# Performance work log

Hardware: AMD Instinct MI355X
Metric: run time of the kernel (lower is better)

The kernel has to match this reference:

```python
import jax, jax.numpy as jnp
import numpy as np

B, T, D, SLB = 65536, 50, 17, 30
DROPOUT_RATE = 0.9  # type-3 Gaussian dropout: mask ~ N(1, sqrt((1-p)/p))


def setup_inputs() -> dict:
    key = jax.random.key(0)
    ks = jax.random.split(key, 9)
    p = float(np.sqrt((1.0 - DROPOUT_RATE) / DROPOUT_RATE))
    return {
        "x": jax.random.normal(ks[0], (B, T, D), jnp.float32),
        "W_ih": jax.random.normal(ks[1], (4 * D, D), jnp.float32) * 0.2,
        "W_hh": jax.random.normal(ks[2], (4 * D, D), jnp.float32) * 0.2,
        "b_ih": jax.random.normal(ks[3], (4 * D,), jnp.float32) * 0.1,
        "b_hh": jax.random.normal(ks[4], (4 * D,), jnp.float32) * 0.1,
        "W_lin": jax.random.normal(ks[5], (D, D), jnp.float32) * 0.2,
        "b_lin": jax.random.normal(ks[6], (D,), jnp.float32) * 0.1,
        "mask_ih": 1.0 + p * jax.random.normal(ks[7], (4 * D, D), jnp.float32),
        "mask_hh": 1.0 + p * jax.random.normal(ks[8], (4 * D, D), jnp.float32),
        "step_look_back": SLB,
    }


def reference(x, W_ih, W_hh, b_ih, b_hh, W_lin, b_lin, mask_ih, mask_hh, step_look_back):
    # Masked weights are constant across timesteps (original recomputes the same
    # product each step); transpose once for right-multiplication.
    Wih_t = (W_ih * mask_ih).T   # [D, 4D]
    Whh_t = (W_hh * mask_hh).T   # [H, 4D]
    Wlin_t = W_lin.T             # [H, C]

    x_tbd = jnp.swapaxes(x, 0, 1)          # [T, B, D]
    Bsz = x.shape[0]
    H = W_hh.shape[1]
    h0 = jnp.zeros((Bsz, H), x.dtype)

    def step(carry, inp):
        h, c, prev_out = carry
        x_t, t = inp
        # Teacher-forced input for t < step_look_back, else feed back prediction.
        xi = jnp.where(t < step_look_back, x_t, prev_out)
        gates = xi @ Wih_t + b_ih + h @ Whh_t + b_hh   # [B, 4H]
        i_g, f_g, g_g, o_g = jnp.split(gates, 4, axis=-1)
        c_new = jax.nn.sigmoid(f_g) * c + jax.nn.sigmoid(i_g) * jnp.tanh(g_g)
        h_new = jax.nn.sigmoid(o_g) * jnp.tanh(c_new)
        out = h_new @ Wlin_t + b_lin                    # [B, C]
        return (h_new, c_new, out), out

    Tlen = x.shape[1]
    _, outs = jax.lax.scan(step, (h0, h0, h0), (x_tbd, jnp.arange(Tlen)))
    # Keep only predicted steps: [T - SLB, B, C] -> [B, T - SLB, C]
    return jnp.swapaxes(outs[step_look_back:], 0, 1)
```

## Files before the change

kernel.cpp:

```cpp
#include <hip/hip_runtime.h>


#define Dn 17
#define Gn 68
#define Tn 50
#define WS 68
#define ZS 51
#define HOFF 34

__device__ __forceinline__ float sigm_(float v) {
    float e = __expf(-v);
    return __builtin_amdgcn_rcpf(1.0f + e);
}
__device__ __forceinline__ float tanh_(float v) {
    float e = __expf(2.0f * v);
    return 1.0f - 2.0f * __builtin_amdgcn_rcpf(e + 1.0f);
}
__device__ __forceinline__ float getc(const float4 v, int c) {
    return c == 0 ? v.x : c == 1 ? v.y : c == 2 ? v.z : v.w;
}
__device__ __forceinline__ void fma4(float4& a, float b, const float4 w) {
    a.x = __builtin_fmaf(b, w.x, a.x);
    a.y = __builtin_fmaf(b, w.y, a.y);
    a.z = __builtin_fmaf(b, w.z, a.z);
    a.w = __builtin_fmaf(b, w.w, a.w);
}

__global__ __launch_bounds__(256, 1)
void lstm_fused(const float* __restrict__ x,
                const float* __restrict__ W_ih, const float* __restrict__ W_hh,
                const float* __restrict__ b_ih, const float* __restrict__ b_hh,
                const float* __restrict__ W_lin, const float* __restrict__ b_lin,
                const float* __restrict__ m_ih, const float* __restrict__ m_hh,
                const int* __restrict__ slb_p, float* __restrict__ out)
{
    __shared__ __align__(16) float sWzT[2 * Dn * WS];
    __shared__ __align__(16) float sCzT[Dn * WS];
    __shared__ __align__(16) float sWlT[Dn * 20];
    __shared__ __align__(16) float sBs[WS];
    __shared__ __align__(16) float sBc[WS];
    __shared__ __align__(16) float sBl[20];
    __shared__ float tmpA[Gn * Dn];
    __shared__ float tmpB[Gn * Dn];
    __shared__ float zbuf[256 * ZS];
    __shared__ float obuf[256 * Dn];

    const int tid = threadIdx.x;
    const int b0  = blockIdx.x * 256;

    for (int i = tid; i < Gn * Dn; i += 256) {
        tmpA[i] = W_ih[i] * m_ih[i];
        tmpB[i] = W_hh[i] * m_hh[i];
    }
    for (int i = tid; i < Dn * 20; i += 256) {
        int k = i / 20, m = i - 20 * k;
        sWlT[i] = (m < Dn) ? W_lin[m * Dn + k] : 0.0f;
    }
    if (tid < WS) sBs[tid] = b_ih[tid] + b_hh[tid];
    if (tid < 20) sBl[tid] = (tid < Dn) ? b_lin[tid] : 0.0f;
    __syncthreads();
    for (int i = tid; i < 2 * Dn * WS; i += 256) {
        int k = i / WS, j = i - WS * k;
        sWzT[i] = (k < Dn) ? tmpA[j * Dn + k] : tmpB[j * Dn + (k - Dn)];
    }
    for (int i = tid; i < Dn * WS; i += 256) {
        int k = i / WS, j = i - WS * k;
        float v = tmpB[j * Dn + k];
        #pragma unroll
        for (int m = 0; m < Dn; ++m) v = __builtin_fmaf(tmpA[j * Dn + m], sWlT[k * 20 + m], v);
        sCzT[i] = v;
    }
    if (tid < Gn) {
        float v = sBs[tid];
        #pragma unroll
        for (int m = 0; m < Dn; ++m) v = __builtin_fmaf(tmpA[tid * Dn + m], sBl[m], v);
        sBc[tid] = v;
    }

    #pragma unroll
    for (int e = 0; e < Dn; ++e) zbuf[tid * ZS + HOFF + e] = 0.0f;
    int offx[17], brow_[17], dcol_[17];
    #pragma unroll
    for (int i = 0; i < 17; ++i) {
        int f = tid + 256 * i;
        int br = f / 17, d = f - 17 * br;
        brow_[i] = br; dcol_[i] = d;
        offx[i] = ((b0 + br) * Tn) * Dn + d;
        zbuf[br * ZS + d] = x[offx[i]];
    }
    __syncthreads();

    const int slb = slb_p[0];
    float c[Dn];
    #pragma unroll
    for (int e = 0; e < Dn; ++e) c[e] = 0.0f;
    const float* zr = &zbuf[tid * ZS];
    const float4* bs4 = (const float4*)sBs;

    for (int t = 0; t < slb; ++t) {
        float gx[17];
        const bool pre = (t + 1 < Tn);
        if (pre) {
            #pragma unroll
            for (int i = 0; i < 17; ++i) gx[i] = x[offx[i] + (t + 1) * Dn];
        }
        float4 acc[17];
        #pragma unroll
        for (int j = 0; j < 17; ++j) acc[j] = bs4[j];
        const int xo = (t & 1) * Dn;
        #pragma unroll 2
        for (int k = 0; k < Dn; ++k) {
            float zk = zr[xo + k];
            const float4* w4 = (const float4*)&sWzT[k * WS];
            #pragma unroll
            for (int j = 0; j < 17; ++j) fma4(acc[j], zk, w4[j]);
        }
        #pragma unroll 2
        for (int k = 0; k < Dn; ++k) {
            float zk = zr[HOFF + k];
            const float4* w4 = (const float4*)&sWzT[(Dn + k) * WS];
            #pragma unroll
            for (int j = 0; j < 17; ++j) fma4(acc[j], zk, w4[j]);
        }
        #pragma unroll
        for (int e = 0; e < Dn; ++e) {
            float gi = getc(acc[e >> 2], e & 3);
            float gf = getc(acc[(Dn + e) >> 2], (Dn + e) & 3);
            float gg = getc(acc[(2 * Dn + e) >> 2], (2 * Dn + e) & 3);
            float go = getc(acc[(3 * Dn + e) >> 2], (3 * Dn + e) & 3);
            float cv = __builtin_fmaf(sigm_(gf), c[e], sigm_(gi) * tanh_(gg));
            c[e] = cv;
            zbuf[tid * ZS + HOFF + e] = sigm_(go) * tanh_(cv);
        }
        if (pre) {
            const int xo2 = ((t + 1) & 1) * Dn;
            #pragma unroll
            for (int i = 0; i < 17; ++i) zbuf[brow_[i] * ZS + xo2 + dcol_[i]] = gx[i];
        }
        __syncthreads();
    }

    const int nout = Tn - slb;
    int offo[17];
    #pragma unroll
    for (int i = 0; i < 17; ++i) offo[i] = ((b0 + brow_[i]) * nout) * Dn + dcol_[i];
    const float4* bc4 = (const float4*)sBc;
    const float4* bl4 = (const float4*)sBl;

    for (int tp = 0; tp < nout; ++tp) {
        float4 acc[17];
        #pragma unroll
        for (int j = 0; j < 17; ++j) acc[j] = bc4[j];
        #pragma unroll 2
        for (int k = 0; k < Dn; ++k) {
            float zk = zr[HOFF + k];
            const float4* w4 = (const float4*)&sCzT[k * WS];
            #pragma unroll
            for (int j = 0; j < 17; ++j) fma4(acc[j], zk, w4[j]);
        }
        float hn[Dn];
        #pragma unroll
        for (int e = 0; e < Dn; ++e) {
            float gi = getc(acc[e >> 2], e & 3);
            float gf = getc(acc[(Dn + e) >> 2], (Dn + e) & 3);
            float gg = getc(acc[(2 * Dn + e) >> 2], (2 * Dn + e) & 3);
            float go = getc(acc[(3 * Dn + e) >> 2], (3 * Dn + e) & 3);
            float cv = __builtin_fmaf(sigm_(gf), c[e], sigm_(gi) * tanh_(gg));
            c[e] = cv;
            hn[e] = sigm_(go) * tanh_(cv);
            zbuf[tid * ZS + HOFF + e] = hn[e];
        }
        float4 o4[5];
        #pragma unroll
        for (int j = 0; j < 5; ++j) o4[j] = bl4[j];
        #pragma unroll
        for (int k = 0; k < Dn; ++k) {
            const float4* w4 = (const float4*)&sWlT[k * 20];
            #pragma unroll
            for (int j = 0; j < 5; ++j) fma4(o4[j], hn[k], w4[j]);
        }
        #pragma unroll
        for (int m = 0; m < Dn; ++m) obuf[tid * Dn + m] = getc(o4[m >> 2], m & 3);
        __syncthreads();
        #pragma unroll
        for (int i = 0; i < 17; ++i) out[offo[i] + tp * Dn] = obuf[tid + 256 * i];
        __syncthreads();
    }
}

extern "C" void kernel_launch(void* const* d_in, const int* in_sizes, int n_in,
                              void* d_out, int out_size, void* d_ws, size_t ws_size,
                              hipStream_t stream) {
    (void)in_sizes; (void)n_in; (void)d_ws; (void)ws_size; (void)out_size;
    const float* x     = (const float*)d_in[0];
    const float* W_ih  = (const float*)d_in[1];
    const float* W_hh  = (const float*)d_in[2];
    const float* b_ih  = (const float*)d_in[3];
    const float* b_hh  = (const float*)d_in[4];
    const float* W_lin = (const float*)d_in[5];
    const float* b_lin = (const float*)d_in[6];
    const float* m_ih  = (const float*)d_in[7];
    const float* m_hh  = (const float*)d_in[8];
    const int*   slb   = (const int*)d_in[9];
    float* out = (float*)d_out;

    lstm_fused<<<dim3(256), dim3(256), 0, stream>>>(
        x, W_ih, W_hh, b_ih, b_hh, W_lin, b_lin, m_ih, m_hh, slb, out);
}
```

Baseline: 766.0 us.

## Split weight prep into setup kernel, read weights from global, keep h in registers

```diff
diff --git a/kernel.cpp b/kernel.cpp
--- a/kernel.cpp
+++ b/kernel.cpp
@@ -4,9 +4,16 @@
 #define Dn 17
 #define Gn 68
 #define Tn 50
-#define WS 68
-#define ZS 51
-#define HOFF 34
+
+#define WZ_OFF 0
+#define CZ_OFF 2312
+#define WL_OFF 3468
+#define BS_OFF 3808
+#define BC_OFF 3876
+#define BL_OFF 3944
+#define WS_FLOATS 3964
+
+__device__ __align__(16) float g_ws[WS_FLOATS];
 
 __device__ __forceinline__ float sigm_(float v) {
     float e = __expf(-v);
@@ -26,101 +33,99 @@
     a.w = __builtin_fmaf(b, w.w, a.w);
 }
 
+__global__ void lstm_setup(const float* __restrict__ W_ih, const float* __restrict__ W_hh,
+                           const float* __restrict__ b_ih, const float* __restrict__ b_hh,
+                           const float* __restrict__ W_lin, const float* __restrict__ b_lin,
+                           const float* __restrict__ m_ih, const float* __restrict__ m_hh)
+{
+    __shared__ float A[Gn * Dn];
+    __shared__ float Bm[Gn * Dn];
+    const int tid = threadIdx.x;
+    for (int i = tid; i < Gn * Dn; i += 256) {
+        A[i]  = W_ih[i] * m_ih[i];
+        Bm[i] = W_hh[i] * m_hh[i];
+    }
+    __syncthreads();
+    for (int i = tid; i < 2 * Dn * Gn; i += 256) {
+        int k = i / Gn, j = i - Gn * k;
+        g_ws[WZ_OFF + i] = (k < Dn) ? A[j * Dn + k] : Bm[j * Dn + (k - Dn)];
+    }
+    for (int i = tid; i < Dn * Gn; i += 256) {
+        int k = i / Gn, j = i - Gn * k;
+        float v = Bm[j * Dn + k];
+        for (int m = 0; m < Dn; ++m) v = __builtin_fmaf(A[j * Dn + m], W_lin[m * Dn + k], v);
+        g_ws[CZ_OFF + i] = v;
+    }
+    for (int i = tid; i < Dn * 20; i += 256) {
+        int k = i / 20, m = i - 20 * k;
+        g_ws[WL_OFF + i] = (m < Dn) ? W_lin[m * Dn + k] : 0.0f;
+    }
+    if (tid < Gn) {
+        float bsv = b_ih[tid] + b_hh[tid];
+        g_ws[BS_OFF + tid] = bsv;
+        float v = bsv;
+        for (int m = 0; m < Dn; ++m) v = __builtin_fmaf(A[tid * Dn + m], b_lin[m], v);
+        g_ws[BC_OFF + tid] = v;
+    }
+    if (tid < 20) g_ws[BL_OFF + tid] = (tid < Dn) ? b_lin[tid] : 0.0f;
+}
+
 __global__ __launch_bounds__(256, 1)
-void lstm_fused(const float* __restrict__ x,
-                const float* __restrict__ W_ih, const float* __restrict__ W_hh,
-                const float* __restrict__ b_ih, const float* __restrict__ b_hh,
-                const float* __restrict__ W_lin, const float* __restrict__ b_lin,
-                const float* __restrict__ m_ih, const float* __restrict__ m_hh,
-                const int* __restrict__ slb_p, float* __restrict__ out)
+void lstm_main(const float* __restrict__ x,
+               const int* __restrict__ slb_p, float* __restrict__ out)
 {
-    __shared__ __align__(16) float sWzT[2 * Dn * WS];
-    __shared__ __align__(16) float sCzT[Dn * WS];
-    __shared__ __align__(16) float sWlT[Dn * 20];
-    __shared__ __align__(16) float sBs[WS];
-    __shared__ __align__(16) float sBc[WS];
-    __shared__ __align__(16) float sBl[20];
-    __shared__ float tmpA[Gn * Dn];
-    __shared__ float tmpB[Gn * Dn];
-    __shared__ float zbuf[256 * ZS];
-    __shared__ float obuf[256 * Dn];
+    __shared__ float xbuf[2][256 * Dn];
 
     const int tid = threadIdx.x;
     const int b0  = blockIdx.x * 256;
 
-    for (int i = tid; i < Gn * Dn; i += 256) {
-        tmpA[i] = W_ih[i] * m_ih[i];
-        tmpB[i] = W_hh[i] * m_hh[i];
-    }
-    for (int i = tid; i < Dn * 20; i += 256) {
-        int k = i / 20, m = i - 20 * k;
-        sWlT[i] = (m < Dn) ? W_lin[m * Dn + k] : 0.0f;
-    }
-    if (tid < WS) sBs[tid] = b_ih[tid] + b_hh[tid];
-    if (tid < 20) sBl[tid] = (tid < Dn) ? b_lin[tid] : 0.0f;
+    const float* __restrict__ wz = g_ws + WZ_OFF;
+    const float* __restrict__ cz = g_ws + CZ_OFF;
+    const float* __restrict__ wl = g_ws + WL_OFF;
+    const float4* bs4 = (const float4*)(g_ws + BS_OFF);
+    const float4* bc4 = (const float4*)(g_ws + BC_OFF);
+    const float4* bl4 = (const float4*)(g_ws + BL_OFF);
+
+    int offx[Dn];
+    #pragma unroll
+    for (int i = 0; i < Dn; ++i) {
+        int f  = tid + 256 * i;
+        int br = f / Dn, d = f - Dn * br;
+        offx[i] = ((b0 + br) * Tn) * Dn + d;
+        xbuf[0][f] = x[offx[i]];
+    }
     __syncthreads();
-    for (int i = tid; i < 2 * Dn * WS; i += 256) {
-        int k = i / WS, j = i - WS * k;
-        sWzT[i] = (k < Dn) ? tmpA[j * Dn + k] : tmpB[j * Dn + (k - Dn)];
-    }
-    for (int i = tid; i < Dn * WS; i += 256) {
-        int k = i / WS, j = i - WS * k;
-        float v = tmpB[j * Dn + k];
-        #pragma unroll
-        for (int m = 0; m < Dn; ++m) v = __builtin_fmaf(tmpA[j * Dn + m], sWlT[k * 20 + m], v);
-        sCzT[i] = v;
-    }
-    if (tid < Gn) {
-        float v = sBs[tid];
-        #pragma unroll
-        for (int m = 0; m < Dn; ++m) v = __builtin_fmaf(tmpA[tid * Dn + m], sBl[m], v);
-        sBc[tid] = v;
-    }
-
+
+    const int slb = slb_p[0];
+    float c[Dn], h[Dn];
     #pragma unroll
-    for (int e = 0; e < Dn; ++e) zbuf[tid * ZS + HOFF + e] = 0.0f;
-    int offx[17], brow_[17], dcol_[17];
-    #pragma unroll
-    for (int i = 0; i < 17; ++i) {
-        int f = tid + 256 * i;
-        int br = f / 17, d = f - 17 * br;
-        brow_[i] = br; dcol_[i] = d;
-        offx[i] = ((b0 + br) * Tn) * Dn + d;
-        zbuf[br * ZS + d] = x[offx[i]];
-    }
-    __syncthreads();
-
-    const int slb = slb_p[0];
-    float c[Dn];
-    #pragma unroll
-    for (int e = 0; e < Dn; ++e) c[e] = 0.0f;
-    const float* zr = &zbuf[tid * ZS];
-    const float4* bs4 = (const float4*)sBs;
+    for (int e = 0; e < Dn; ++e) { c[e] = 0.0f; h[e] = 0.0f; }
 
     for (int t = 0; t < slb; ++t) {
-        float gx[17];
-        const bool pre = (t + 1 < Tn);
+        const bool pre = (t + 1 < slb);
+        float gx[Dn];
         if (pre) {
             #pragma unroll
-            for (int i = 0; i < 17; ++i) gx[i] = x[offx[i] + (t + 1) * Dn];
-        }
-        float4 acc[17];
-        #pragma unroll
-        for (int j = 0; j < 17; ++j) acc[j] = bs4[j];
-        const int xo = (t & 1) * Dn;
-        #pragma unroll 2
-        for (int k = 0; k < Dn; ++k) {
-            float zk = zr[xo + k];
-            const float4* w4 = (const float4*)&sWzT[k * WS];
-            #pragma unroll
-            for (int j = 0; j < 17; ++j) fma4(acc[j], zk, w4[j]);
-        }
-        #pragma unroll 2
-        for (int k = 0; k < Dn; ++k) {
-            float zk = zr[HOFF + k];
-            const float4* w4 = (const float4*)&sWzT[(Dn + k) * WS];
-            #pragma unroll
-            for (int j = 0; j < 17; ++j) fma4(acc[j], zk, w4[j]);
+            for (int i = 0; i < Dn; ++i) gx[i] = x[offx[i] + (t + 1) * Dn];
+        }
+        float4 acc[Dn];
+        #pragma unroll
+        for (int j = 0; j < Dn; ++j) acc[j] = bs4[j];
+
+        const float* xr = &xbuf[t & 1][tid * Dn];
+        #pragma unroll
+        for (int k = 0; k < Dn; ++k) {
+            float zk = xr[k];
+            const float4* w4 = (const float4*)(wz + k * Gn);
+            #pragma unroll
+            for (int j = 0; j < Dn; ++j) fma4(acc[j], zk, w4[j]);
+        }
+        #pragma unroll
+        for (int k = 0; k < Dn; ++k) {
+            float zk = h[k];
+            const float4* w4 = (const float4*)(wz + (Dn + k) * Gn);
+            #pragma unroll
+            for (int j = 0; j < Dn; ++j) fma4(acc[j], zk, w4[j]);
         }
         #pragma unroll
         for (int e = 0; e < Dn; ++e) {
@@ -130,35 +135,29 @@
             float go = getc(acc[(3 * Dn + e) >> 2], (3 * Dn + e) & 3);
             float cv = __builtin_fmaf(sigm_(gf), c[e], sigm_(gi) * tanh_(gg));
             c[e] = cv;
-            zbuf[tid * ZS + HOFF + e] = sigm_(go) * tanh_(cv);
+            h[e] = sigm_(go) * tanh_(cv);
         }
         if (pre) {
-            const int xo2 = ((t + 1) & 1) * Dn;
-            #pragma unroll
-            for (int i = 0; i < 17; ++i) zbuf[brow_[i] * ZS + xo2 + dcol_[i]] = gx[i];
+            const int p = (t + 1) & 1;
+            #pragma unroll
+            for (int i = 0; i < Dn; ++i) xbuf[p][tid + 256 * i] = gx[i];
         }
         __syncthreads();
     }
 
-    const int nout = Tn - slb;
-    int offo[17];
-    #pragma unroll
-    for (int i = 0; i < 17; ++i) offo[i] = ((b0 + brow_[i]) * nout) * Dn + dcol_[i];
-    const float4* bc4 = (const float4*)sBc;
-    const float4* bl4 = (const float4*)sBl;
-
+    const int nout  = Tn - slb;
+    const int obase = (b0 + tid) * nout * Dn;
     for (int tp = 0; tp < nout; ++tp) {
-        float4 acc[17];
-        #pragma unroll
-        for (int j = 0; j < 17; ++j) acc[j] = bc4[j];
-        #pragma unroll 2
-        for (int k = 0; k < Dn; ++k) {
-            float zk = zr[HOFF + k];
-            const float4* w4 = (const float4*)&sCzT[k * WS];
-            #pragma unroll
-            for (int j = 0; j < 17; ++j) fma4(acc[j], zk, w4[j]);
-        }
-        float hn[Dn];
+        float4 acc[Dn];
+        #pragma unroll
+        for (int j = 0; j < Dn; ++j) acc[j] = bc4[j];
+        #pragma unroll
+        for (int k = 0; k < Dn; ++k) {
+            float zk = h[k];
+            const float4* w4 = (const float4*)(cz + k * Gn);
+            #pragma unroll
+            for (int j = 0; j < Dn; ++j) fma4(acc[j], zk, w4[j]);
+        }
         #pragma unroll
         for (int e = 0; e < Dn; ++e) {
             float gi = getc(acc[e >> 2], e & 3);
@@ -167,31 +166,27 @@
             float go = getc(acc[(3 * Dn + e) >> 2], (3 * Dn + e) & 3);
             float cv = __builtin_fmaf(sigm_(gf), c[e], sigm_(gi) * tanh_(gg));
             c[e] = cv;
-            hn[e] = sigm_(go) * tanh_(cv);
-            zbuf[tid * ZS + HOFF + e] = hn[e];
+            h[e] = sigm_(go) * tanh_(cv);
         }
         float4 o4[5];
         #pragma unroll
         for (int j = 0; j < 5; ++j) o4[j] = bl4[j];
         #pragma unroll
         for (int k = 0; k < Dn; ++k) {
-            const float4* w4 = (const float4*)&sWlT[k * 20];
-            #pragma unroll
-            for (int j = 0; j < 5; ++j) fma4(o4[j], hn[k], w4[j]);
-        }
-        #pragma unroll
-        for (int m = 0; m < Dn; ++m) obuf[tid * Dn + m] = getc(o4[m >> 2], m & 3);
-        __syncthreads();
-        #pragma unroll
-        for (int i = 0; i < 17; ++i) out[offo[i] + tp * Dn] = obuf[tid + 256 * i];
-        __syncthreads();
+            const float4* w4 = (const float4*)(wl + k * 20);
+            #pragma unroll
+            for (int j = 0; j < 5; ++j) fma4(o4[j], h[k], w4[j]);
+        }
+        float* op = out + obase + tp * Dn;
+        #pragma unroll
+        for (int m = 0; m < Dn; ++m) op[m] = getc(o4[m >> 2], m & 3);
     }
 }
 
 extern "C" void kernel_launch(void* const* d_in, const int* in_sizes, int n_in,
                               void* d_out, int out_size, void* d_ws, size_t ws_size,
                               hipStream_t stream) {
-    (void)in_sizes; (void)n_in; (void)d_ws; (void)ws_size; (void)out_size;
+    (void)in_sizes; (void)n_in; (void)ws_size; (void)out_size; (void)d_ws;
     const float* x     = (const float*)d_in[0];
     const float* W_ih  = (const float*)d_in[1];
     const float* W_hh  = (const float*)d_in[2];
@@ -204,6 +199,7 @@
     const int*   slb   = (const int*)d_in[9];
     float* out = (float*)d_out;
 
-    lstm_fused<<<dim3(256), dim3(256), 0, stream>>>(
-        x, W_ih, W_hh, b_ih, b_hh, W_lin, b_lin, m_ih, m_hh, slb, out);
-}
+    lstm_setup<<<dim3(1), dim3(256), 0, stream>>>(
+        W_ih, W_hh, b_ih, b_hh, W_lin, b_lin, m_ih, m_hh);
+    lstm_main<<<dim3(256), dim3(256), 0, stream>>>(x, slb, out);
+}
```

After: 1.105 ms. 1.44x slower.

## Process two batch rows per thread and keep hidden state in registers

Applied to the files above, without the earlier changes.

```diff
diff --git a/kernel.cpp b/kernel.cpp
--- a/kernel.cpp
+++ b/kernel.cpp
@@ -5,8 +5,9 @@
 #define Gn 68
 #define Tn 50
 #define WS 68
-#define ZS 51
-#define HOFF 34
+#define ZS 35
+#define NT 128
+#define NB 256
 
 __device__ __forceinline__ float sigm_(float v) {
     float e = __expf(-v);
@@ -26,7 +27,7 @@
     a.w = __builtin_fmaf(b, w.w, a.w);
 }
 
-__global__ __launch_bounds__(256, 1)
+__global__ __launch_bounds__(NT, 1)
 void lstm_fused(const float* __restrict__ x,
                 const float* __restrict__ W_ih, const float* __restrict__ W_hh,
                 const float* __restrict__ b_ih, const float* __restrict__ b_hh,
@@ -42,28 +43,28 @@
     __shared__ __align__(16) float sBl[20];
     __shared__ float tmpA[Gn * Dn];
     __shared__ float tmpB[Gn * Dn];
-    __shared__ float zbuf[256 * ZS];
-    __shared__ float obuf[256 * Dn];
+    __shared__ float zbuf[NB * ZS];
+    __shared__ float obuf[NB * Dn];
 
     const int tid = threadIdx.x;
-    const int b0  = blockIdx.x * 256;
-
-    for (int i = tid; i < Gn * Dn; i += 256) {
+    const int b0  = blockIdx.x * NB;
+
+    for (int i = tid; i < Gn * Dn; i += NT) {
         tmpA[i] = W_ih[i] * m_ih[i];
         tmpB[i] = W_hh[i] * m_hh[i];
     }
-    for (int i = tid; i < Dn * 20; i += 256) {
+    for (int i = tid; i < Dn * 20; i += NT) {
         int k = i / 20, m = i - 20 * k;
         sWlT[i] = (m < Dn) ? W_lin[m * Dn + k] : 0.0f;
     }
     if (tid < WS) sBs[tid] = b_ih[tid] + b_hh[tid];
     if (tid < 20) sBl[tid] = (tid < Dn) ? b_lin[tid] : 0.0f;
     __syncthreads();
-    for (int i = tid; i < 2 * Dn * WS; i += 256) {
+    for (int i = tid; i < 2 * Dn * WS; i += NT) {
         int k = i / WS, j = i - WS * k;
         sWzT[i] = (k < Dn) ? tmpA[j * Dn + k] : tmpB[j * Dn + (k - Dn)];
     }
-    for (int i = tid; i < Dn * WS; i += 256) {
+    for (int i = tid; i < Dn * WS; i += NT) {
         int k = i / WS, j = i - WS * k;
         float v = tmpB[j * Dn + k];
         #pragma unroll
@@ -78,112 +79,140 @@
     }
 
     #pragma unroll
-    for (int e = 0; e < Dn; ++e) zbuf[tid * ZS + HOFF + e] = 0.0f;
-    int offx[17], brow_[17], dcol_[17];
+    for (int i = 0; i < 34; ++i) {
+        int f  = tid + NT * i;
+        int br = f / Dn, d = f - Dn * br;
+        zbuf[br * ZS + d] = x[(b0 + br) * (Tn * Dn) + d];
+    }
+    __syncthreads();
+
+    const int slb = slb_p[0];
+    float c0_[Dn], c1_[Dn], h0_[Dn], h1_[Dn];
     #pragma unroll
-    for (int i = 0; i < 17; ++i) {
-        int f = tid + 256 * i;
-        int br = f / 17, d = f - 17 * br;
-        brow_[i] = br; dcol_[i] = d;
-        offx[i] = ((b0 + br) * Tn) * Dn + d;
-        zbuf[br * ZS + d] = x[offx[i]];
-    }
-    __syncthreads();
-
-    const int slb = slb_p[0];
-    float c[Dn];
-    #pragma unroll
-    for (int e = 0; e < Dn; ++e) c[e] = 0.0f;
-    const float* zr = &zbuf[tid * ZS];
+    for (int e = 0; e < Dn; ++e) { c0_[e] = 0.0f; c1_[e] = 0.0f; h0_[e] = 0.0f; h1_[e] = 0.0f; }
+
+    const float* zr0 = &zbuf[tid * ZS];
+    const float* zr1 = &zbuf[(tid + NT) * ZS];
     const float4* bs4 = (const float4*)sBs;
 
     for (int t = 0; t < slb; ++t) {
-        float gx[17];
-        const bool pre = (t + 1 < Tn);
+        const bool pre = (t + 1 < slb);
+        float gx[34];
         if (pre) {
             #pragma unroll
-            for (int i = 0; i < 17; ++i) gx[i] = x[offx[i] + (t + 1) * Dn];
-        }
-        float4 acc[17];
-        #pragma unroll
-        for (int j = 0; j < 17; ++j) acc[j] = bs4[j];
+            for (int i = 0; i < 34; ++i) {
+                int f  = tid + NT * i;
+                int br = f / Dn, d = f - Dn * br;
+                gx[i] = x[(b0 + br) * (Tn * Dn) + (t + 1) * Dn + d];
+            }
+        }
+        float4 a0[Dn], a1[Dn];
+        #pragma unroll
+        for (int j = 0; j < Dn; ++j) { a0[j] = bs4[j]; a1[j] = bs4[j]; }
         const int xo = (t & 1) * Dn;
         #pragma unroll 2
         for (int k = 0; k < Dn; ++k) {
-            float zk = zr[xo + k];
+            float z0 = zr0[xo + k], z1 = zr1[xo + k];
             const float4* w4 = (const float4*)&sWzT[k * WS];
             #pragma unroll
-            for (int j = 0; j < 17; ++j) fma4(acc[j], zk, w4[j]);
+            for (int j = 0; j < Dn; ++j) { float4 w = w4[j]; fma4(a0[j], z0, w); fma4(a1[j], z1, w); }
         }
         #pragma unroll 2
         for (int k = 0; k < Dn; ++k) {
-            float zk = zr[HOFF + k];
+            float z0 = h0_[k], z1 = h1_[k];
             const float4* w4 = (const float4*)&sWzT[(Dn + k) * WS];
             #pragma unroll
-            for (int j = 0; j < 17; ++j) fma4(acc[j], zk, w4[j]);
-        }
-        #pragma unroll
-        for (int e = 0; e < Dn; ++e) {
-            float gi = getc(acc[e >> 2], e & 3);
-            float gf = getc(acc[(Dn + e) >> 2], (Dn + e) & 3);
-            float gg = getc(acc[(2 * Dn + e) >> 2], (2 * Dn + e) & 3);
-            float go = getc(acc[(3 * Dn + e) >> 2], (3 * Dn + e) & 3);
-            float cv = __builtin_fmaf(sigm_(gf), c[e], sigm_(gi) * tanh_(gg));
-            c[e] = cv;
-            zbuf[tid * ZS + HOFF + e] = sigm_(go) * tanh_(cv);
+            for (int j = 0; j < Dn; ++j) { float4 w = w4[j]; fma4(a0[j], z0, w); fma4(a1[j], z1, w); }
+        }
+        #pragma unroll
+        for (int e = 0; e < Dn; ++e) {
+            float gi = getc(a0[e >> 2], e & 3);
+            float gf = getc(a0[(Dn + e) >> 2], (Dn + e) & 3);
+            float gg = getc(a0[(2 * Dn + e) >> 2], (2 * Dn + e) & 3);
+            float go = getc(a0[(3 * Dn + e) >> 2], (3 * Dn + e) & 3);
+            float cv = __builtin_fmaf(sigm_(gf), c0_[e], sigm_(gi) * tanh_(gg));
+            c0_[e] = cv;
+            h0_[e] = sigm_(go) * tanh_(cv);
+        }
+        #pragma unroll
+        for (int e = 0; e < Dn; ++e) {
+            float gi = getc(a1[e >> 2], e & 3);
+            float gf = getc(a1[(Dn + e) >> 2], (Dn + e) & 3);
+            float gg = getc(a1[(2 * Dn + e) >> 2], (2 * Dn + e) & 3);
+            float go = getc(a1[(3 * Dn + e) >> 2], (3 * Dn + e) & 3);
+            float cv = __builtin_fmaf(sigm_(gf), c1_[e], sigm_(gi) * tanh_(gg));
+            c1_[e] = cv;
+            h1_[e] = sigm_(go) * tanh_(cv);
         }
         if (pre) {
             const int xo2 = ((t + 1) & 1) * Dn;
             #pragma unroll
-            for (int i = 0; i < 17; ++i) zbuf[brow_[i] * ZS + xo2 + dcol_[i]] = gx[i];
+            for (int i = 0; i < 34; ++i) {
+                int f  = tid + NT * i;
+                int br = f / Dn, d = f - Dn * br;
+                zbuf[br * ZS + xo2 + d] = gx[i];
+            }
         }
         __syncthreads();
     }
 
     const int nout = Tn - slb;
-    int offo[17];
-    #pragma unroll
-    for (int i = 0; i < 17; ++i) offo[i] = ((b0 + brow_[i]) * nout) * Dn + dcol_[i];
+    const int ostr = nout * Dn;
     const float4* bc4 = (const float4*)sBc;
     const float4* bl4 = (const float4*)sBl;
 
     for (int tp = 0; tp < nout; ++tp) {
-        float4 acc[17];
-        #pragma unroll
-        for (int j = 0; j < 17; ++j) acc[j] = bc4[j];
+        float4 a0[Dn], a1[Dn];
+        #pragma unroll
+        for (int j = 0; j < Dn; ++j) { a0[j] = bc4[j]; a1[j] = bc4[j]; }
         #pragma unroll 2
         for (int k = 0; k < Dn; ++k) {
-            float zk = zr[HOFF + k];
+            float z0 = h0_[k], z1 = h1_[k];
             const float4* w4 = (const float4*)&sCzT[k * WS];
             #pragma unroll
-            for (int j = 0; j < 17; ++j) fma4(acc[j], zk, w4[j]);
-        }
-        float hn[Dn];
-        #pragma unroll
-        for (int e = 0; e < Dn; ++e) {
-            float gi = getc(acc[e >> 2], e & 3);
-            float gf = getc(acc[(Dn + e) >> 2], (Dn + e) & 3);
-            float gg = getc(acc[(2 * Dn + e) >> 2], (2 * Dn + e) & 3);
-            float go = getc(acc[(3 * Dn + e) >> 2], (3 * Dn + e) & 3);
-            float cv = __builtin_fmaf(sigm_(gf), c[e], sigm_(gi) * tanh_(gg));
-            c[e] = cv;
-            hn[e] = sigm_(go) * tanh_(cv);
-            zbuf[tid * ZS + HOFF + e] = hn[e];
-        }
-        float4 o4[5];
-        #pragma unroll
-        for (int j = 0; j < 5; ++j) o4[j] = bl4[j];
+            for (int j = 0; j < Dn; ++j) { float4 w = w4[j]; fma4(a0[j], z0, w); fma4(a1[j], z1, w); }
+        }
+        #pragma unroll
+        for (int e = 0; e < Dn; ++e) {
+            float gi = getc(a0[e >> 2], e & 3);
+            float gf = getc(a0[(Dn + e) >> 2], (Dn + e) & 3);
+            float gg = getc(a0[(2 * Dn + e) >> 2], (2 * Dn + e) & 3);
+            float go = getc(a0[(3 * Dn + e) >> 2], (3 * Dn + e) & 3);
+            float cv = __builtin_fmaf(sigm_(gf), c0_[e], sigm_(gi) * tanh_(gg));
+            c0_[e] = cv;
+            h0_[e] = sigm_(go) * tanh_(cv);
+        }
+        #pragma unroll
+        for (int e = 0; e < Dn; ++e) {
+            float gi = getc(a1[e >> 2], e & 3);
+            float gf = getc(a1[(Dn + e) >> 2], (Dn + e) & 3);
+            float gg = getc(a1[(2 * Dn + e) >> 2], (2 * Dn + e) & 3);
+            float go = getc(a1[(3 * Dn + e) >> 2], (3 * Dn + e) & 3);
+            float cv = __builtin_fmaf(sigm_(gf), c1_[e], sigm_(gi) * tanh_(gg));
+            c1_[e] = cv;
+            h1_[e] = sigm_(go) * tanh_(cv);
+        }
+        float4 o0[5], o1[5];
+        #pragma unroll
+        for (int j = 0; j < 5; ++j) { o0[j] = bl4[j]; o1[j] = bl4[j]; }
         #pragma unroll
         for (int k = 0; k < Dn; ++k) {
             const float4* w4 = (const float4*)&sWlT[k * 20];
             #pragma unroll
-            for (int j = 0; j < 5; ++j) fma4(o4[j], hn[k], w4[j]);
-        }
-        #pragma unroll
-        for (int m = 0; m < Dn; ++m) obuf[tid * Dn + m] = getc(o4[m >> 2], m & 3);
+            for (int j = 0; j < 5; ++j) { float4 w = w4[j]; fma4(o0[j], h0_[k], w); fma4(o1[j], h1_[k], w); }
+        }
+        #pragma unroll
+        for (int m = 0; m < Dn; ++m) {
+            obuf[tid * Dn + m]        = getc(o0[m >> 2], m & 3);
+            obuf[(tid + NT) * Dn + m] = getc(o1[m >> 2], m & 3);
+        }
         __syncthreads();
         #pragma unroll
-        for (int i = 0; i < 17; ++i) out[offo[i] + tp * Dn] = obuf[tid + 256 * i];
+        for (int i = 0; i < 34; ++i) {
+            int f  = tid + NT * i;
+            int br = f / Dn, d = f - Dn * br;
+            out[(b0 + br) * ostr + tp * Dn + d] = obuf[f];
+        }
         __syncthreads();
     }
 }
@@ -204,6 +233,6 @@
     const int*   slb   = (const int*)d_in[9];
     float* out = (float*)d_out;
 
-    lstm_fused<<<dim3(256), dim3(256), 0, stream>>>(
+    lstm_fused<<<dim3(256), dim3(NT), 0, stream>>>(
         x, W_ih, W_hh, b_ih, b_hh, W_lin, b_lin, m_ih, m_hh, slb, out);
 }
```

Result: slower. 1.034 ms (+35.0%).
